# Optimization experiments

Hardware: AMD Instinct MI355X
Metric: run time of the kernel (lower is better)

## Reference

```python
import jax, jax.numpy as jnp
import numpy as np

EMB = 1024
HEADS = 16
S = EMB // HEADS  # 64
B, T = 2, 2048


def setup_inputs() -> dict:
    key = jax.random.key(0)
    ks = jax.random.split(key, 5)
    x = jax.random.normal(ks[0], (B, T, EMB), dtype=jnp.float32)
    Wk = jax.random.normal(ks[1], (S, S), dtype=jnp.float32) * (1.0 / np.sqrt(S))
    Wq = jax.random.normal(ks[2], (S, S), dtype=jnp.float32) * (1.0 / np.sqrt(S))
    Wv = jax.random.normal(ks[3], (S, S), dtype=jnp.float32) * (1.0 / np.sqrt(S))
    Wu = jax.random.normal(ks[4], (EMB, EMB), dtype=jnp.float32) * (1.0 / np.sqrt(EMB))
    bu = jnp.zeros((EMB,), dtype=jnp.float32)
    return {"x": x, "Wk": Wk, "Wq": Wq, "Wv": Wv, "Wu": Wu, "bu": bu}


def reference(x, Wk, Wq, Wv, Wu, bu):
    b, t, e = x.shape
    h, s = HEADS, e // HEADS
    xh = x.reshape(b, t, h, s)
    # torch Linear: y = x @ W.T (per-head projection, weights shared across heads)
    keys = jnp.einsum('bths,os->btho', xh, Wk)
    queries = jnp.einsum('bths,os->btho', xh, Wq)
    values = jnp.einsum('bths,os->btho', xh, Wv)
    scale = e ** (-0.25)
    queries = queries * scale
    keys = keys * scale
    # [b, h, t_q, t_k] full score matrix (as in the original bmm)
    dot = jnp.einsum('bqhd,bkhd->bhqk', queries, keys)
    attn = jax.nn.softmax(dot, axis=-1)
    out = jnp.einsum('bhqk,bkhd->bqhd', attn, values).reshape(b, t, e)
    return out @ Wu.T + bu
```

## Files before the change

kernel.cpp:

```cpp
#include <hip/hip_runtime.h>
#include <hip/hip_bf16.h>
#include <stdint.h>

#define TT   2048
#define EMB  1024
#define SDIM 64
#define KVB  128
#define NIT  (TT / KVB)
#define LOG2E 1.4426950408889634f

typedef float f32x2  __attribute__((ext_vector_type(2)));
typedef float f32x4  __attribute__((ext_vector_type(4)));
typedef float f32x16 __attribute__((ext_vector_type(16)));
typedef short short8 __attribute__((ext_vector_type(8)));
typedef unsigned short ushort4v __attribute__((ext_vector_type(4)));
typedef unsigned int uint2v __attribute__((ext_vector_type(2)));
typedef unsigned int uint4v __attribute__((ext_vector_type(4)));

__device__ __forceinline__ ushort f2bf(float f) {
    uint32_t u = __builtin_bit_cast(uint32_t, f);
    u += 0x7FFFu + ((u >> 16) & 1u);
    return (ushort)(u >> 16);
}

__device__ __forceinline__ short8 cvt8(const float* p) {
    f32x4 a = *(const f32x4*)p;
    f32x4 b = *(const f32x4*)(p + 4);
    short8 r;
    r[0] = (short)f2bf(a[0]); r[1] = (short)f2bf(a[1]);
    r[2] = (short)f2bf(a[2]); r[3] = (short)f2bf(a[3]);
    r[4] = (short)f2bf(b[0]); r[5] = (short)f2bf(b[1]);
    r[6] = (short)f2bf(b[2]); r[7] = (short)f2bf(b[3]);
    return r;
}

__device__ __forceinline__ void gload16(const void* g, void* l) {
    __builtin_amdgcn_global_load_lds((const __attribute__((address_space(1))) uint32_t*)g,
                                     (__attribute__((address_space(3))) uint32_t*)l, 16, 0, 0);
}
__device__ __forceinline__ uint pkbf(float a, float b) {
    uint d; asm("v_cvt_pk_bf16_f32 %0, %1, %2" : "=v"(d) : "v"(a), "v"(b)); return d;
}
__device__ __forceinline__ void swap32(uint& a, uint& b) {
    asm volatile("s_nop 1\n\tv_permlane32_swap_b32 %0, %1" : "+v"(a), "+v"(b));
}
__device__ __forceinline__ float xhadd(float x) {
    uint a = __builtin_bit_cast(uint, x), o;
    asm volatile("v_mov_b32 %0, %1\n\ts_nop 3\n\tv_permlane32_swap_b32 %0, %1"
                 : "=&v"(o), "+v"(a));
    return __builtin_bit_cast(float, o) + __builtin_bit_cast(float, a);
}

__global__ __launch_bounds__(256) void cvt_w(const float* __restrict__ Wk, const float* __restrict__ Wq,
                                             const float* __restrict__ Wv, const float* __restrict__ Wu,
                                             ushort* __restrict__ Wk16, ushort* __restrict__ Wq16,
                                             ushort* __restrict__ Wv16, ushort* __restrict__ Wu16) {
    int i = blockIdx.x * 256 + threadIdx.x;
    Wu16[i] = f2bf(Wu[i]);
    if (i < 4096) {
        Wk16[i] = f2bf(Wk[i]);
        Wq16[i] = f2bf(Wq[i] * (0.03125f * LOG2E));
        Wv16[i] = f2bf(Wv[i]);
    }
}

__global__ __launch_bounds__(256) void qkv(const float* __restrict__ x,
                                           const ushort* __restrict__ Wk16, const ushort* __restrict__ Wq16,
                                           const ushort* __restrict__ Wv16,
                                           ushort* __restrict__ Qw, ushort* __restrict__ Kw, ushort* __restrict__ Vt) {
    const int tid = threadIdx.x;
    const int wave = tid >> 6, lane = tid & 63;
    const int c = lane & 15, g = lane >> 4;
    const int rblk = (blockIdx.x * 4 + wave) * 16;
    const int bh = rblk >> 11;
    const int tbase = rblk & (TT - 1);
    const int b = bh >> 4, h = bh & 15;

    const float* xrow = x + ((size_t)(b * TT + tbase + c) * EMB + h * SDIM);
    short8 a[2];
#pragma unroll
    for (int ks = 0; ks < 2; ++ks) a[ks] = cvt8(xrow + 32 * ks + 8 * g);

    f32x4 aq[4], ak[4], av[4];
#pragma unroll
    for (int n = 0; n < 4; ++n) { aq[n] = 0.f; ak[n] = 0.f; av[n] = 0.f; }

#pragma unroll
    for (int n = 0; n < 4; ++n) {
#pragma unroll
        for (int ks = 0; ks < 2; ++ks) {
            const size_t wo = (size_t)(16 * n + c) * SDIM + 32 * ks + 8 * g;
            short8 bq = *(const short8*)(Wq16 + wo);
            short8 bk = *(const short8*)(Wk16 + wo);
            short8 bv = *(const short8*)(Wv16 + wo);
            aq[n] = __builtin_amdgcn_mfma_f32_16x16x32_bf16(a[ks], bq, aq[n], 0, 0, 0);
            ak[n] = __builtin_amdgcn_mfma_f32_16x16x32_bf16(a[ks], bk, ak[n], 0, 0, 0);
            av[n] = __builtin_amdgcn_mfma_f32_16x16x32_bf16(a[ks], bv, av[n], 0, 0, 0);
        }
    }
    const size_t hb = (size_t)bh * TT * SDIM;
#pragma unroll
    for (int n = 0; n < 4; ++n) {
#pragma unroll
        for (int i = 0; i < 4; ++i) {
            const size_t o = hb + (size_t)(tbase + 4 * g + i) * SDIM + 16 * n + c;
            Qw[o] = f2bf(aq[n][i]);
            Kw[o] = f2bf(ak[n][i]);
        }
        ushort4v vp;
#pragma unroll
        for (int i = 0; i < 4; ++i) vp[i] = f2bf(av[n][i]);
        *(ushort4v*)(Vt + hb + (size_t)(16 * n + c) * TT + tbase + 4 * g) = vp;
    }
}

__global__ __launch_bounds__(512, 4) void attn(const ushort* __restrict__ Qw, const ushort* __restrict__ Kw,
                                               const ushort* __restrict__ Vt, ushort* __restrict__ AO) {
    __shared__ ushort smem[4][8192];

    const int tid = threadIdx.x;
    const int wv = tid >> 6, lane = tid & 63;
    const int q = lane & 31, hi = lane >> 5;
    const int qg = wv & 3, kh = wv >> 2;
    const int wo = kh * 64;

    const int wg = blockIdx.x;
    const int xcd = wg & 7, slot = wg >> 3;
    const int bh = xcd * 4 + (slot >> 4);
    const int qt = slot & 15;
    const int b = bh >> 4, h = bh & 15;
    const int qrowW = qt * 128 + qg * 32;
    const size_t base = (size_t)bh * TT * SDIM;

    short8 qa[4];
    const ushort* Qp = Qw + base + (size_t)(qrowW + q) * SDIM + 8 * hi;
#pragma unroll
    for (int sb = 0; sb < 4; ++sb) qa[sb] = *(const short8*)(Qp + 16 * sb);

    f32x16 a0v = 0.f, a1v = 0.f;
    float lsum = 0.f;

    const int krow = lane >> 3;
    const ushort* Ks = Kw + base + (size_t)(wv * 8 + krow) * SDIM + (((lane & 7) ^ krow) * 8);
    const int vrow = wv * 4 + (lane >> 4);
    const ushort* Vs = Vt + base + (size_t)vrow * TT + (((lane & 15) ^ (vrow & 15)) * 8);

#define STAGE(kvb, buf) { \
    char* kb = (char*)&smem[(buf)][0] + wv * 1024;      \
    char* vb = (char*)&smem[2 + (buf)][0] + wv * 1024;  \
    _Pragma("unroll")                                    \
    for (int p = 0; p < 2; ++p) {                        \
        gload16(Ks + (kvb) * 64 + p * 4096, kb + p * 8192); \
        gload16(Vs + (kvb) + p * 32 * TT,   vb + p * 8192); \
    } }

    STAGE(0, 0);
    __syncthreads();

    const int kmask = (q & 7) << 4;
    const int vmask = q & 15;
    int cur = 0;
    for (int kt = 0; kt < NIT; ++kt) {
        if (kt < NIT - 1) STAGE((kt + 1) * KVB, cur ^ 1);
        const char* Kc = (const char*)&smem[cur][0];
        const char* Vc = (const char*)&smem[2 + cur][0];

        f32x16 s0 = 0.f, s1 = 0.f;
#pragma unroll
        for (int sb = 0; sb < 4; ++sb) {
            const int off = (32 * sb + 16 * hi) ^ kmask;
            short8 k0 = *(const short8*)(Kc + (wo + q) * 128 + off);
            s0 = __builtin_amdgcn_mfma_f32_32x32x16_bf16(k0, qa[sb], s0, 0, 0, 0);
            short8 k1 = *(const short8*)(Kc + (wo + 32 + q) * 128 + off);
            s1 = __builtin_amdgcn_mfma_f32_32x32x16_bf16(k1, qa[sb], s1, 0, 0, 0);
        }

        float r0 = 0.f, r1 = 0.f;
#pragma unroll
        for (int i = 0; i < 16; ++i) { float p = __builtin_amdgcn_exp2f(s0[i]); s0[i] = p; r0 += p; }
#pragma unroll
        for (int i = 0; i < 16; ++i) { float p = __builtin_amdgcn_exp2f(s1[i]); s1[i] = p; r1 += p; }
        lsum += r0 + r1;

        short8 pb0, pb1, pb2, pb3;
#define RP(sv, pa_, pb_) { \
        uint u0 = pkbf(sv[0], sv[1]),   u1 = pkbf(sv[2], sv[3]);   \
        uint u2 = pkbf(sv[4], sv[5]),   u3 = pkbf(sv[6], sv[7]);   \
        swap32(u0, u2); swap32(u1, u3);                            \
        uint4v ta = {u0, u1, u2, u3}; pa_ = __builtin_bit_cast(short8, ta); \
        uint u4 = pkbf(sv[8], sv[9]),   u5 = pkbf(sv[10], sv[11]); \
        uint u6 = pkbf(sv[12], sv[13]), u7 = pkbf(sv[14], sv[15]); \
        swap32(u4, u6); swap32(u5, u7);                            \
        uint4v tb = {u4, u5, u6, u7}; pb_ = __builtin_bit_cast(short8, tb); }
        RP(s0, pb0, pb1) RP(s1, pb2, pb3)
#undef RP

#define PV(kstep, pbk) { \
        const int u = ((2 * (kstep) + hi + kh * 8) ^ vmask) << 4;          \
        short8 v0 = *(const short8*)(Vc + q * 256 + u);                    \
        a0v = __builtin_amdgcn_mfma_f32_32x32x16_bf16(v0, pbk, a0v, 0, 0, 0); \
        short8 v1 = *(const short8*)(Vc + (32 + q) * 256 + u);             \
        a1v = __builtin_amdgcn_mfma_f32_32x32x16_bf16(v1, pbk, a1v, 0, 0, 0); }
        PV(0, pb0) PV(1, pb1) PV(2, pb2) PV(3, pb3)
#undef PV

        __syncthreads();
        cur ^= 1;
    }
#undef STAGE

    f32x2* ob = (f32x2*)&smem[0][0];
    float* lb = (float*)&smem[0][0] + 8192;
    const int mb = qg * 1024 + lane;
    if (kh) {
#pragma unroll
        for (int j = 0; j < 8; ++j) { f32x2 t = {a0v[2 * j], a0v[2 * j + 1]}; ob[mb + j * 64] = t; }
#pragma unroll
        for (int j = 0; j < 8; ++j) { f32x2 t = {a1v[2 * j], a1v[2 * j + 1]}; ob[mb + (8 + j) * 64] = t; }
        lb[qg * 64 + lane] = lsum;
    }
    __syncthreads();
    if (kh) return;

#pragma unroll
    for (int j = 0; j < 8; ++j) { f32x2 t = ob[mb + j * 64];       a0v[2 * j] += t[0]; a0v[2 * j + 1] += t[1]; }
#pragma unroll
    for (int j = 0; j < 8; ++j) { f32x2 t = ob[mb + (8 + j) * 64]; a1v[2 * j] += t[0]; a1v[2 * j + 1] += t[1]; }
    lsum += lb[qg * 64 + lane];

    const float l_i = xhadd(lsum);
    char* scrB = (char*)&smem[0][0] + 40960 + qg * 4096;
    const int eswz = (q & 7) << 4;
    float inv = 1.f / l_i;
#pragma unroll
    for (int sb2 = 0; sb2 < 2; ++sb2) {
#pragma unroll
        for (int bq = 0; bq < 4; ++bq) {
            float v0 = (sb2 ? a1v[4 * bq + 0] : a0v[4 * bq + 0]) * inv;
            float v1 = (sb2 ? a1v[4 * bq + 1] : a0v[4 * bq + 1]) * inv;
            float v2 = (sb2 ? a1v[4 * bq + 2] : a0v[4 * bq + 2]) * inv;
            float v3 = (sb2 ? a1v[4 * bq + 3] : a0v[4 * bq + 3]) * inv;
            uint2v d; d[0] = pkbf(v0, v1); d[1] = pkbf(v2, v3);
            int s0e = 8 * bq + 4 * hi + 32 * sb2;
            *(uint2v*)(scrB + q * 128 + ((s0e * 2) ^ eswz)) = d;
        }
    }
    asm volatile("s_waitcnt lgkmcnt(0)" ::: "memory");
    ushort* AOp = AO + (size_t)(b * TT + qrowW + q) * EMB + h * SDIM + 32 * hi;
#pragma unroll
    for (int jj = 0; jj < 4; ++jj) {
        short8 o = *(const short8*)(scrB + q * 128 + ((64 * hi + 16 * jj) ^ eswz));
        *(short8*)(AOp + 8 * jj) = o;
    }
}

__global__ __launch_bounds__(512) void oproj(const ushort* __restrict__ AO, const ushort* __restrict__ Wu16,
                                             const float* __restrict__ bu, float* __restrict__ out) {
    __shared__ ushort Ab[2][128 * 64];
    __shared__ ushort Bb[2][128 * 64];
    const int tid = threadIdx.x;
    const int wv = tid >> 6, lane = tid & 63;
    const int c = lane & 15, g = lane >> 4;
    const int wr = wv >> 1, wc = wv & 1;
    const int rblk = blockIdx.x * 128, nblk = blockIdx.y * 128;

    const int row0 = tid >> 3;
    const int col0 = ((tid & 7) ^ (row0 & 7)) * 8;
    const ushort* As0 = AO   + (size_t)(rblk + row0) * EMB + col0;
    const ushort* As1 = AO   + (size_t)(rblk + row0 + 64) * EMB + col0;
    const ushort* Bs0 = Wu16 + (size_t)(nblk + row0) * EMB + col0;
    const ushort* Bs1 = Wu16 + (size_t)(nblk + row0 + 64) * EMB + col0;
    const int l0 = wv * 512, l1 = 4096 + wv * 512;

    f32x4 acc[2][4];
#pragma unroll
    for (int m = 0; m < 2; ++m)
#pragma unroll
        for (int n = 0; n < 4; ++n) acc[m][n] = 0.f;

    gload16(As0, &Ab[0][l0]); gload16(As1, &Ab[0][l1]);
    gload16(Bs0, &Bb[0][l0]); gload16(Bs1, &Bb[0][l1]);
    __syncthreads();

    const int swzA = (c & 7) << 4;
    int cur = 0;
    for (int kt = 0; kt < 16; ++kt) {
        if (kt < 15) {
            const int k0 = (kt + 1) * 64;
            gload16(As0 + k0, &Ab[cur ^ 1][l0]); gload16(As1 + k0, &Ab[cur ^ 1][l1]);
            gload16(Bs0 + k0, &Bb[cur ^ 1][l0]); gload16(Bs1 + k0, &Bb[cur ^ 1][l1]);
        }
        const char* Ac = (const char*)&Ab[cur][0];
        const char* Bc = (const char*)&Bb[cur][0];
#pragma unroll
        for (int kb = 0; kb < 2; ++kb) {
            short8 am[2], bn[4];
#pragma unroll
            for (int m = 0; m < 2; ++m)
                am[m] = *(const short8*)(Ac + (wr * 32 + 16 * m + c) * 128 + ((64 * kb + 16 * g) ^ swzA));
#pragma unroll
            for (int n = 0; n < 4; ++n)
                bn[n] = *(const short8*)(Bc + (wc * 64 + 16 * n + c) * 128 + ((64 * kb + 16 * g) ^ swzA));
#pragma unroll
            for (int m = 0; m < 2; ++m)
#pragma unroll
                for (int n = 0; n < 4; ++n)
                    acc[m][n] = __builtin_amdgcn_mfma_f32_16x16x32_bf16(am[m], bn[n], acc[m][n], 0, 0, 0);
        }
        __syncthreads();
        cur ^= 1;
    }
#pragma unroll
    for (int m = 0; m < 2; ++m)
#pragma unroll
        for (int n = 0; n < 4; ++n) {
            float bias = bu[nblk + wc * 64 + 16 * n + c];
#pragma unroll
            for (int i = 0; i < 4; ++i)
                out[(size_t)(rblk + wr * 32 + 16 * m + 4 * g + i) * EMB + nblk + wc * 64 + 16 * n + c] =
                    acc[m][n][i] + bias;
        }
}

extern "C" void kernel_launch(void* const* d_in, const int* in_sizes, int n_in,
                              void* d_out, int out_size, void* d_ws, size_t ws_size,
                              hipStream_t stream) {
    const float* x  = (const float*)d_in[0];
    const float* Wk = (const float*)d_in[1];
    const float* Wq = (const float*)d_in[2];
    const float* Wv = (const float*)d_in[3];
    const float* Wu = (const float*)d_in[4];
    const float* bu = (const float*)d_in[5];
    float* out = (float*)d_out;

    char* ws = (char*)d_ws;
    const size_t MB = 1024u * 1024u;
    ushort* Qw   = (ushort*)(ws);
    ushort* Kw   = (ushort*)(ws + 8 * MB);
    ushort* Vt   = (ushort*)(ws + 16 * MB);
    ushort* AO   = (ushort*)(ws + 24 * MB);
    ushort* Wu16 = (ushort*)(ws + 32 * MB);
    ushort* Wk16 = (ushort*)(ws + 34 * MB);
    ushort* Wq16 = Wk16 + 4096;
    ushort* Wv16 = Wk16 + 8192;

    cvt_w<<<dim3(4096), dim3(256), 0, stream>>>(Wk, Wq, Wv, Wu, Wk16, Wq16, Wv16, Wu16);
    qkv<<<dim3(1024), dim3(256), 0, stream>>>(x, Wk16, Wq16, Wv16, Qw, Kw, Vt);
    attn<<<dim3(512), dim3(512), 0, stream>>>(Qw, Kw, Vt, AO);
    oproj<<<dim3(32, 8), dim3(512), 0, stream>>>(AO, Wu16, bu, out);
}
```

Baseline: 84.58 us.

## Fold Wu conversion into qkv launch and remap oproj tiles per XCD

The large Wu fp32-to-bf16 conversion moves out of the small cvt_w kernel into 256 extra blocks of the qkv launch. Those blocks use vectorized 16-element loads and stores, and they run alongside the QKV projection blocks instead of as a separate serialized kernel, so cvt_w now only converts the three 64x64 weights. The oproj grid is flattened to 1D and remapped so each XCD handles a contiguous group of row tiles across all column tiles, aiming for better L2 reuse of A rows. The fused qkv launch adds some tail imbalance.

```diff
diff --git a/kernel.cpp b/kernel.cpp
--- a/kernel.cpp
+++ b/kernel.cpp
@@ -52,23 +52,33 @@
 }
 
 __global__ __launch_bounds__(256) void cvt_w(const float* __restrict__ Wk, const float* __restrict__ Wq,
-                                             const float* __restrict__ Wv, const float* __restrict__ Wu,
+                                             const float* __restrict__ Wv,
                                              ushort* __restrict__ Wk16, ushort* __restrict__ Wq16,
-                                             ushort* __restrict__ Wv16, ushort* __restrict__ Wu16) {
+                                             ushort* __restrict__ Wv16) {
     int i = blockIdx.x * 256 + threadIdx.x;
-    Wu16[i] = f2bf(Wu[i]);
-    if (i < 4096) {
-        Wk16[i] = f2bf(Wk[i]);
-        Wq16[i] = f2bf(Wq[i] * (0.03125f * LOG2E));
-        Wv16[i] = f2bf(Wv[i]);
-    }
+    Wk16[i] = f2bf(Wk[i]);
+    Wq16[i] = f2bf(Wq[i] * (0.03125f * LOG2E));
+    Wv16[i] = f2bf(Wv[i]);
 }
 
 __global__ __launch_bounds__(256) void qkv(const float* __restrict__ x,
                                            const ushort* __restrict__ Wk16, const ushort* __restrict__ Wq16,
                                            const ushort* __restrict__ Wv16,
-                                           ushort* __restrict__ Qw, ushort* __restrict__ Kw, ushort* __restrict__ Vt) {
+                                           ushort* __restrict__ Qw, ushort* __restrict__ Kw, ushort* __restrict__ Vt,
+                                           const float* __restrict__ Wu, ushort* __restrict__ Wu16) {
     const int tid = threadIdx.x;
+    if (blockIdx.x >= 1024) {
+        const int gbase = ((blockIdx.x - 1024) * 256 + tid) * 16;
+#pragma unroll
+        for (int j = 0; j < 4; ++j) {
+            f32x4 v = *(const f32x4*)(Wu + gbase + 4 * j);
+            ushort4v o;
+#pragma unroll
+            for (int e = 0; e < 4; ++e) o[e] = f2bf(v[e]);
+            *(ushort4v*)(Wu16 + gbase + 4 * j) = o;
+        }
+        return;
+    }
     const int wave = tid >> 6, lane = tid & 63;
     const int c = lane & 15, g = lane >> 4;
     const int rblk = (blockIdx.x * 4 + wave) * 16;
@@ -262,7 +272,10 @@
     const int wv = tid >> 6, lane = tid & 63;
     const int c = lane & 15, g = lane >> 4;
     const int wr = wv >> 1, wc = wv & 1;
-    const int rblk = blockIdx.x * 128, nblk = blockIdx.y * 128;
+    const int wg = blockIdx.x;
+    const int xcd = wg & 7, i6 = wg >> 3;
+    const int rblk = (xcd * 4 + (i6 >> 3)) * 128;
+    const int nblk = (i6 & 7) * 128;
 
     const int row0 = tid >> 3;
     const int col0 = ((tid & 7) ^ (row0 & 7)) * 8;
@@ -344,8 +357,8 @@
     ushort* Wq16 = Wk16 + 4096;
     ushort* Wv16 = Wk16 + 8192;
 
-    cvt_w<<<dim3(4096), dim3(256), 0, stream>>>(Wk, Wq, Wv, Wu, Wk16, Wq16, Wv16, Wu16);
-    qkv<<<dim3(1024), dim3(256), 0, stream>>>(x, Wk16, Wq16, Wv16, Qw, Kw, Vt);
+    cvt_w<<<dim3(16), dim3(256), 0, stream>>>(Wk, Wq, Wv, Wk16, Wq16, Wv16);
+    qkv<<<dim3(1280), dim3(256), 0, stream>>>(x, Wk16, Wq16, Wv16, Qw, Kw, Vt, Wu, Wu16);
     attn<<<dim3(512), dim3(512), 0, stream>>>(Qw, Kw, Vt, AO);
-    oproj<<<dim3(32, 8), dim3(512), 0, stream>>>(AO, Wu16, bu, out);
-}
+    oproj<<<dim3(256), dim3(512), 0, stream>>>(AO, Wu16, bu, out);
+}
```

After: 84.79 us. About the same (+0.2%).
